# Kernel optimization log

Measured on AMD Instinct MI355X. Metric: run time of the kernel, lower is better.

## Reference

```python
import jax, jax.numpy as jnp
import numpy as np

N = 100000   # nodes
E = 300000   # edges
D = 256      # emb_dim
L = 5        # num_layers
SELF_LOOP_BOND_TYPE = 4
BN_EPS = 1e-5


def setup_inputs() -> dict:
    key = jax.random.key(0)
    ks = jax.random.split(key, 12)
    s = 0.05
    x = jax.random.randint(ks[0], (N, 2), 0, 3)
    edge_index = jax.random.randint(ks[1], (2, E), 0, N)
    edge_attr = jax.random.randint(ks[2], (E, 2), 0, 3)
    x_emb1 = jax.random.normal(ks[3], (120, D), dtype=jnp.float32) * s
    x_emb2 = jax.random.normal(ks[4], (3, D), dtype=jnp.float32) * s
    edge_emb1 = jax.random.normal(ks[5], (L, 6, D), dtype=jnp.float32) * s
    edge_emb2 = jax.random.normal(ks[6], (L, 3, D), dtype=jnp.float32) * s
    W1 = jax.random.normal(ks[7], (L, D, 2 * D), dtype=jnp.float32) * (1.0 / np.sqrt(D))
    b1 = jnp.zeros((L, 2 * D), dtype=jnp.float32)
    W2 = jax.random.normal(ks[8], (L, 2 * D, D), dtype=jnp.float32) * (1.0 / np.sqrt(2 * D))
    b2 = jnp.zeros((L, D), dtype=jnp.float32)
    bn_gamma = jnp.ones((L - 1, D), dtype=jnp.float32)
    bn_beta = jnp.zeros((L - 1, D), dtype=jnp.float32)
    return dict(x=x, edge_index=edge_index, edge_attr=edge_attr,
                x_emb1=x_emb1, x_emb2=x_emb2,
                edge_emb1=edge_emb1, edge_emb2=edge_emb2,
                W1=W1, b1=b1, W2=W2, b2=b2,
                bn_gamma=bn_gamma, bn_beta=bn_beta)


def reference(x, edge_index, edge_attr, x_emb1, x_emb2, edge_emb1, edge_emb2,
              W1, b1, W2, b2, bn_gamma, bn_beta):
    n = x.shape[0]
    loop = jnp.arange(n)
    # add_self_loops: append (i, i) for every node
    src = jnp.concatenate([edge_index[0], loop])  # [E+N]
    dst = jnp.concatenate([edge_index[1], loop])  # [E+N]
    # self-loop edge_attr = (bond_type=4, direction=0)
    self_attr = jnp.concatenate([
        jnp.full((n, 1), SELF_LOOP_BOND_TYPE, dtype=edge_attr.dtype),
        jnp.zeros((n, 1), dtype=edge_attr.dtype)], axis=1)
    ea = jnp.concatenate([edge_attr, self_attr], axis=0)  # [E+N, 2]

    out = x_emb1[x[:, 0]] + x_emb2[x[:, 1]]  # [N, D]
    for l in range(L):
        e_emb = edge_emb1[l][ea[:, 0]] + edge_emb2[l][ea[:, 1]]  # [E+N, D]
        msg = out[src] + e_emb                                   # gather + message
        agg = jax.ops.segment_sum(msg, dst, num_segments=n)      # scatter-add
        h = jax.nn.relu(agg @ W1[l] + b1[l]) @ W2[l] + b2[l]     # GIN MLP
        if l < L - 1:
            mean = h.mean(axis=0)
            var = h.var(axis=0)  # biased var, matches torch BN training
            h = (h - mean) * jax.lax.rsqrt(var + BN_EPS) * bn_gamma[l] + bn_beta[l]
            h = jax.nn.relu(h)
        out = h
    return out
```

## Files before the change

kernel.cpp:

```cpp
#include <hip/hip_runtime.h>

typedef unsigned short u16;
typedef unsigned int u32;

#define DD 256
#define PLCAP 1536

typedef short  s16x8 __attribute__((ext_vector_type(8)));
typedef short  s16x4 __attribute__((ext_vector_type(4)));
typedef float  f32x4 __attribute__((ext_vector_type(4)));
typedef float  f32x16 __attribute__((ext_vector_type(16)));

__device__ __forceinline__ float b2f(u16 u){
  union { u32 i; float f; } c; c.i = ((u32)u) << 16; return c.f;
}
__device__ __forceinline__ u16 f2b(float f){
  union { float f; u32 i; } c; c.f = f;
  u32 b = c.i + 0x7FFFu + ((c.i >> 16) & 1u);
  return (u16)(b >> 16);
}

__global__ void NodeEncoder_72971494359603_kernel(){}

__global__ void probe_dtype(const u32* w, u32* flag){
  if (threadIdx.x == 0 && blockIdx.x == 0){
    int cnt = 0;
    for (int i = 0; i < 256; i++){
      u32 low = w[i] & 0xFFFFu;
      u32 e = (low >> 7) & 0xFFu;
      if (e >= 0x60u && e <= 0x7Eu) cnt++;
    }
    *flag = (cnt >= 192) ? 1u : 0u;
  }
}

__global__ void cvt_in(const void* src, u16* dst, int n, const u32* flag){
  int i = blockIdx.x * 256 + threadIdx.x;
  if (i < n){
    if (*flag){
      dst[i] = ((const u16*)src)[i];
    } else {
      dst[i] = f2b(((const float*)src)[i]);
    }
  }
}

__global__ void store_out(const u16* h, void* dout, int n, const u32* flag){
  int i = blockIdx.x * 256 + threadIdx.x;
  if (i < n){
    if (*flag){
      ((u16*)dout)[i] = h[i];
    } else {
      ((float*)dout)[i] = b2f(h[i]);
    }
  }
}

__global__ void zero_int(int* p, int n){
  int i = blockIdx.x * 256 + threadIdx.x;
  if (i < n) p[i] = 0;
}

__global__ void build_table(const u16* ee1, const u16* ee2, u16* TBL){
  int b = blockIdx.x;
  int l = b / 18, c = b % 18, a = c / 3, bb = c % 3;
  int j = threadIdx.x;
  TBL[b * DD + j] = f2b(b2f(ee1[(l * 6 + a) * DD + j]) + b2f(ee2[(l * 3 + bb) * DD + j]));
}

__global__ void hist_kernel(const int* dst, int* counts, int E){
  int e = blockIdx.x * 256 + threadIdx.x;
  if (e < E) atomicAdd(&counts[dst[e]], 1);
}

__global__ void scan_sums(const int* counts, int* bsum, int N){
  __shared__ int red[256];
  int tid = threadIdx.x;
  int base = blockIdx.x * 1024;
  int s = 0;
  for (int i = tid; i < 1024; i += 256){
    int g = base + i;
    if (g < N) s += counts[g];
  }
  red[tid] = s;
  __syncthreads();
  for (int off = 128; off > 0; off >>= 1){
    if (tid < off) red[tid] += red[tid + off];
    __syncthreads();
  }
  if (tid == 0) bsum[blockIdx.x] = red[0];
}

__global__ void scan_top(int* bsum, int nb){
  if (threadIdx.x == 0 && blockIdx.x == 0){
    int acc = 0;
    for (int i = 0; i < nb; i++){ int t = bsum[i]; bsum[i] = acc; acc += t; }
  }
}

__global__ void scan_block(const int* counts, const int* bsum,
                           int* offsets, int* cursor, int N){
  __shared__ int tsum[256];
  int b = blockIdx.x;
  int tid = threadIdx.x;
  int base = b * 1024;
  int v0, v1, v2, v3;
  int g = base + tid * 4;
  v0 = (g + 0 < N) ? counts[g + 0] : 0;
  v1 = (g + 1 < N) ? counts[g + 1] : 0;
  v2 = (g + 2 < N) ? counts[g + 2] : 0;
  v3 = (g + 3 < N) ? counts[g + 3] : 0;
  tsum[tid] = v0 + v1 + v2 + v3;
  __syncthreads();
  for (int off = 1; off < 256; off <<= 1){
    int t = (tid >= off) ? tsum[tid - off] : 0;
    __syncthreads();
    tsum[tid] += t;
    __syncthreads();
  }
  int excl = (tid == 0 ? 0 : tsum[tid - 1]) + bsum[b];
  if (g + 0 < N){ offsets[g + 0] = excl; cursor[g + 0] = excl; } excl += v0;
  if (g + 1 < N){ offsets[g + 1] = excl; cursor[g + 1] = excl; } excl += v1;
  if (g + 2 < N){ offsets[g + 2] = excl; cursor[g + 2] = excl; } excl += v2;
  if (g + 3 < N){ offsets[g + 3] = excl; cursor[g + 3] = excl; }
}

__global__ void fill_csr(const int* ei, const int* ea, int* cursor,
                         int* payload, int E){
  int e = blockIdx.x * 256 + threadIdx.x;
  if (e < E){
    int d = ei[E + e];
    int pos = atomicAdd(&cursor[d], 1);
    int a = ea[2 * e], bb = ea[2 * e + 1];
    payload[pos] = ei[e] | ((a * 3 + bb) << 17);
  }
}

__global__ void node_embed(const int* x, const u16* xe1, const u16* xe2,
                           u16* out, int N){
  int idx = blockIdx.x * 256 + threadIdx.x;
  if (idx < N * DD){
    int n = idx >> 8, j = idx & 255;
    int x0 = x[2 * n], x1 = x[2 * n + 1];
    out[idx] = f2b(b2f(xe1[x0 * DD + j]) + b2f(xe2[x1 * DD + j]));
  }
}

__global__ void pack_B(const u16* __restrict__ W0, u16* __restrict__ Wp0, int K, int Nc){
  const u16* W = W0 + (size_t)blockIdx.y * K * Nc;
  u16* Wp = Wp0 + (size_t)blockIdx.y * K * Nc;
  int idx = blockIdx.x * 256 + threadIdx.x;
  int lane = idx & 63;
  int t = idx >> 6;
  int nk = K >> 4;
  int kstep = t % nk, cblk = t / nk;
  if (cblk >= (Nc >> 5)) return;
  int col = cblk * 32 + (lane & 31);
  int krow = kstep * 16 + (lane >> 5) * 8;
  u16* dst = Wp + (size_t)idx * 8;
#pragma unroll
  for (int e = 0; e < 8; e++)
    dst[e] = W[(size_t)(krow + e) * Nc + col];
}

__global__ __launch_bounds__(512, 4)
void layer_fused(const u16* __restrict__ feat, const u16* __restrict__ TBL,
                 const int* __restrict__ offsets, const int* __restrict__ counts,
                 const int* __restrict__ payload,
                 const u16* __restrict__ Wp1, const u16* __restrict__ bias1,
                 const u16* __restrict__ Wp2, const u16* __restrict__ bias2,
                 u16* __restrict__ H, float* __restrict__ partial, int npart, int M,
                 const float* __restrict__ sums, const u16* __restrict__ gamma,
                 const u16* __restrict__ beta, float invN, int apply_bn){
  __shared__ __align__(16) u16 As[64 * 256];
  __shared__ __align__(16) u16 Ms[2][64 * 128];
  u16* T = (u16*)Ms;
  int* PL = (int*)((char*)Ms + 10240);
  int tid = threadIdx.x, lane = tid & 63, wave = tid >> 6;
  int wr = wave >> 2, wc = wave & 3;
  int row0 = blockIdx.x * 64;
  int l31 = lane & 31, lhi = lane >> 5;

  {
    u32* Tw = (u32*)T;
    const u32* Gw = (const u32*)TBL;
    for (int i = tid; i < 18 * DD / 2; i += 512) Tw[i] = Gw[i];
  }
  int nlast = row0 + 63; if (nlast > M - 1) nlast = M - 1;
  int e_start = offsets[row0];
  int e_total = offsets[nlast] + counts[nlast] - e_start;
  for (int i = tid; i < e_total && i < PLCAP; i += 512) PL[i] = payload[e_start + i];
  __syncthreads();

  {
    int c4 = lane * 4;
    float sc[4], sh[4];
    if (apply_bn){
#pragma unroll
      for (int e = 0; e < 4; e++){
        int j = c4 + e;
        float mean = sums[j] * invN;
        float var = sums[DD + j] * invN - mean * mean;
        if (var < 0.f) var = 0.f;
        float scl = rsqrtf(var + 1e-5f) * b2f(gamma[j]);
        sc[e] = scl; sh[e] = b2f(beta[j]) - mean * scl;
      }
    } else {
#pragma unroll
      for (int e = 0; e < 4; e++){ sc[e] = 1.f; sh[e] = 0.f; }
    }
    int rbase = wave * 8;
    int offs[8], cnts[8]; s16x4 sv[8];
#pragma unroll
    for (int u = 0; u < 8; u++){
      int n = row0 + rbase + u; if (n > M - 1) n = M - 1;
      offs[u] = offsets[n]; cnts[u] = counts[n];
      sv[u] = *(const s16x4*)(feat + (size_t)n * DD + c4);
    }
    s16x4 tb = *(const s16x4*)(T + 12 * DD + c4);
#pragma unroll
    for (int up = 0; up < 4; up++){
      float a0[4], a1[4];
#pragma unroll
      for (int h = 0; h < 2; h++){
        float* a = h ? a1 : a0;
        s16x4 svv = sv[up * 2 + h];
#pragma unroll
        for (int j = 0; j < 4; j++){
          float v = b2f((u16)svv[j]) * sc[j] + sh[j];
          if (apply_bn) v = fmaxf(v, 0.f);
          a[j] = v + b2f((u16)tb[j]);
        }
      }
      int e0 = offs[up * 2],     c0 = cnts[up * 2],     i0 = 0;
      int e1 = offs[up * 2 + 1], c1 = cnts[up * 2 + 1], i1 = 0;
      while (i0 < c0 || i1 < c1){
        int b0 = c0 - i0; if (b0 > 4) b0 = 4; if (b0 < 0) b0 = 0;
        int b1 = c1 - i1; if (b1 > 4) b1 = 4; if (b1 < 0) b1 = 0;
        int pls0[4], pls1[4]; s16x4 rv0[4], rv1[4];
#pragma unroll
        for (int i = 0; i < 4; i++){
          if (i < b0){
            int idx = e0 + i0 + i - e_start;
            pls0[i] = (idx < PLCAP) ? PL[idx] : payload[e0 + i0 + i];
          }
          if (i < b1){
            int idx = e1 + i1 + i - e_start;
            pls1[i] = (idx < PLCAP) ? PL[idx] : payload[e1 + i1 + i];
          }
        }
#pragma unroll
        for (int i = 0; i < 4; i++)
          if (i < b0) rv0[i] = *(const s16x4*)(feat + (size_t)(pls0[i] & 0x1FFFF) * DD + c4);
#pragma unroll
        for (int i = 0; i < 4; i++)
          if (i < b1) rv1[i] = *(const s16x4*)(feat + (size_t)(pls1[i] & 0x1FFFF) * DD + c4);
#pragma unroll
        for (int i = 0; i < 4; i++){
          if (i < b0){
            s16x4 tv = *(const s16x4*)(T + (pls0[i] >> 17) * DD + c4);
#pragma unroll
            for (int j = 0; j < 4; j++){
              float w = b2f((u16)rv0[i][j]) * sc[j] + sh[j];
              if (apply_bn) w = fmaxf(w, 0.f);
              a0[j] += w + b2f((u16)tv[j]);
            }
          }
          if (i < b1){
            s16x4 tv = *(const s16x4*)(T + (pls1[i] >> 17) * DD + c4);
#pragma unroll
            for (int j = 0; j < 4; j++){
              float w = b2f((u16)rv1[i][j]) * sc[j] + sh[j];
              if (apply_bn) w = fmaxf(w, 0.f);
              a1[j] += w + b2f((u16)tv[j]);
            }
          }
        }
        i0 += b0; i1 += b1;
      }
#pragma unroll
      for (int h = 0; h < 2; h++){
        float* a = h ? a1 : a0;
        int r = rbase + up * 2 + h;
        s16x4 o;
        o[0] = (short)f2b(a[0]); o[1] = (short)f2b(a[1]);
        o[2] = (short)f2b(a[2]); o[3] = (short)f2b(a[3]);
        int byteo = r * 512 + (((lane >> 1) ^ (r & 31)) << 4) + ((lane & 1) << 3);
        *(s16x4*)((char*)As + byteo) = o;
      }
    }
  }
  __syncthreads();

  f32x16 acc2[2];
#pragma unroll
  for (int n = 0; n < 2; n++)
#pragma unroll
    for (int i = 0; i < 16; i++) acc2[n][i] = 0.f;
  f32x16 acc1;

  auto G1 = [&](int cc){
    f32x16 a1;
#pragma unroll
    for (int i = 0; i < 16; i++) a1[i] = 0.f;
    int arow = wr * 32 + l31;
    int cb = cc * 4 + wc;
#pragma unroll
    for (int ks = 0; ks < 16; ks++){
      int slot = (ks * 2 + lhi) ^ (arow & 31);
      s16x8 af = *(const s16x8*)((const char*)As + arow * 512 + (slot << 4));
      s16x8 bf = *(const s16x8*)(Wp1 + (((size_t)cb * 16 + ks) * 64 + lane) * 8);
      a1 = __builtin_amdgcn_mfma_f32_32x32x16_bf16(af, bf, a1, 0, 0, 0);
    }
    acc1 = a1;
  };
  auto WMS = [&](int cc, int buf){
    char* ms = (char*)Ms[buf];
    int col = wc * 32 + l31;
    float bv = b2f(bias1[cc * 128 + col]);
#pragma unroll
    for (int reg = 0; reg < 16; reg++){
      int mrow = wr * 32 + (reg & 3) + 8 * (reg >> 2) + 4 * lhi;
      float v = fmaxf(acc1[reg] + bv, 0.f);
      int slot = (col >> 3) ^ (mrow & 15);
      *(u16*)(ms + mrow * 256 + (slot << 4) + (col & 7) * 2) = f2b(v);
    }
  };

  G1(0);
  WMS(0, 0);
  __syncthreads();

#pragma unroll
  for (int c = 0; c < 4; c++){
    const char* ms = (const char*)Ms[c & 1];
    int mrow = wr * 32 + l31;
#pragma unroll
    for (int ks = 0; ks < 8; ks++){
      int slot = (ks * 2 + lhi) ^ (mrow & 15);
      s16x8 mf = *(const s16x8*)(ms + mrow * 256 + (slot << 4));
#pragma unroll
      for (int n = 0; n < 2; n++){
        int cb2 = wc * 2 + n;
        s16x8 wf = *(const s16x8*)(Wp2 + (((size_t)cb2 * 32 + c * 8 + ks) * 64 + lane) * 8);
        acc2[n] = __builtin_amdgcn_mfma_f32_32x32x16_bf16(mf, wf, acc2[n], 0, 0, 0);
      }
    }
    if (c < 3){
      G1(c + 1);
      WMS(c + 1, (c + 1) & 1);
      __syncthreads();
    }
  }

#pragma unroll
  for (int n = 0; n < 2; n++){
    int col = wc * 64 + n * 32 + l31;
    float bv = b2f(bias2[col]);
#pragma unroll
    for (int reg = 0; reg < 16; reg++){
      int row = wr * 32 + (reg & 3) + 8 * (reg >> 2) + 4 * lhi;
      int slot = (col >> 3) ^ (row & 31);
      *(u16*)((char*)As + row * 512 + (slot << 4) + (col & 7) * 2) = f2b(acc2[n][reg] + bv);
    }
  }
  __syncthreads();

  float s[8], q[8];
#pragma unroll
  for (int e = 0; e < 8; e++){ s[e] = 0.f; q[e] = 0.f; }
  int sl = tid & 31;
#pragma unroll
  for (int p = 0; p < 4; p++){
    int r = p * 16 + (tid >> 5);
    s16x8 v = *(const s16x8*)((const char*)As + r * 512 + ((sl ^ (r & 31)) << 4));
    int gr = row0 + r;
    if (gr < M){
      *(s16x8*)(H + (size_t)gr * DD + sl * 8) = v;
      if (partial){
#pragma unroll
        for (int e = 0; e < 8; e++){
          float f = b2f((u16)v[e]);
          s[e] += f; q[e] += f * f;
        }
      }
    }
  }
  if (partial){
#pragma unroll
    for (int e = 0; e < 8; e++){
      s[e] += __shfl_xor(s[e], 32);
      q[e] += __shfl_xor(q[e], 32);
    }
    __syncthreads();
    float* redS = (float*)Ms;
    float* redQ = redS + 8 * 256;
    if (lane < 32){
#pragma unroll
      for (int e = 0; e < 8; e++){
        redS[wave * 256 + sl * 8 + e] = s[e];
        redQ[wave * 256 + sl * 8 + e] = q[e];
      }
    }
    __syncthreads();
    if (tid < 256){
      float a = 0.f, b = 0.f;
#pragma unroll
      for (int w = 0; w < 8; w++){ a += redS[w * 256 + tid]; b += redQ[w * 256 + tid]; }
      partial[(size_t)blockIdx.x * DD + tid] = a;
      partial[(size_t)(npart + blockIdx.x) * DD + tid] = b;
    }
  }
}

__global__ void bn_reduce(const float* __restrict__ partial, float* __restrict__ sums,
                          int npart){
  int b = blockIdx.x, which = b >> 3, jg = b & 7;
  int t = threadIdx.x;
  int j = jg * 32 + (t >> 3);
  int li = t & 7;
  float s = 0.f;
  for (int i = li; i < npart; i += 8)
    s += partial[(size_t)(which * npart + i) * DD + j];
  s += __shfl_xor(s, 1); s += __shfl_xor(s, 2); s += __shfl_xor(s, 4);
  if (li == 0) sums[which * DD + j] = s;
}

extern "C" void kernel_launch(void* const* d_in, const int* in_sizes, int n_in,
                              void* d_out, int out_size, void* d_ws, size_t ws_size,
                              hipStream_t stream){
  (void)n_in; (void)out_size; (void)ws_size;
  const int* x    = (const int*)d_in[0];
  const int* ei   = (const int*)d_in[1];
  const int* ea   = (const int*)d_in[2];
  const void* xe1 = d_in[3];
  const void* xe2 = d_in[4];
  const void* ee1 = d_in[5];
  const void* ee2 = d_in[6];
  const void* W1  = d_in[7];
  const void* b1  = d_in[8];
  const void* W2  = d_in[9];
  const void* b2  = d_in[10];
  const void* gam = d_in[11];
  const void* bet = d_in[12];

  int N = in_sizes[0] / 2;
  int E = in_sizes[1] / 2;
  int NB = (N + 1023) / 1024;
  const int L = 5;
  int nblk = (N + 63) / 64;
  int npart = nblk;

  char* base = (char*)d_ws;
  size_t off = 0;
  u32* flag    = (u32*)(base + off);   off += 256;
  u16* TBL     = (u16*)(base + off);   off += ((size_t)L * 18 * DD * 2 + 255) & ~(size_t)255;
  int* counts  = (int*)(base + off);   off += ((size_t)N * 4 + 255) & ~(size_t)255;
  int* offsets = (int*)(base + off);   off += ((size_t)N * 4 + 255) & ~(size_t)255;
  int* cursor  = (int*)(base + off);   off += ((size_t)N * 4 + 255) & ~(size_t)255;
  int* bsum    = (int*)(base + off);   off += ((size_t)NB * 4 + 255) & ~(size_t)255;
  int* payload = (int*)(base + off);   off += ((size_t)E * 4 + 255) & ~(size_t)255;
  float* part  = (float*)(base + off); off += ((size_t)2 * npart * DD * 4 + 255) & ~(size_t)255;
  float* sums  = (float*)(base + off); off += ((size_t)2 * DD * 4 + 255) & ~(size_t)255;
  u16* wx1  = (u16*)(base + off); off += ((size_t)120 * DD * 2 + 255) & ~(size_t)255;
  u16* wx2  = (u16*)(base + off); off += ((size_t)3 * DD * 2 + 255) & ~(size_t)255;
  u16* wee1 = (u16*)(base + off); off += ((size_t)L * 6 * DD * 2 + 255) & ~(size_t)255;
  u16* wee2 = (u16*)(base + off); off += ((size_t)L * 3 * DD * 2 + 255) & ~(size_t)255;
  u16* wW1  = (u16*)(base + off); off += ((size_t)L * DD * 2 * DD * 2 + 255) & ~(size_t)255;
  u16* wb1  = (u16*)(base + off); off += ((size_t)L * 2 * DD * 2 + 255) & ~(size_t)255;
  u16* wW2  = (u16*)(base + off); off += ((size_t)L * 2 * DD * DD * 2 + 255) & ~(size_t)255;
  u16* wb2  = (u16*)(base + off); off += ((size_t)L * DD * 2 + 255) & ~(size_t)255;
  u16* wgam = (u16*)(base + off); off += ((size_t)(L - 1) * DD * 2 + 255) & ~(size_t)255;
  u16* wbet = (u16*)(base + off); off += ((size_t)(L - 1) * DD * 2 + 255) & ~(size_t)255;
  u16* Wp1  = (u16*)(base + off); off += ((size_t)L * DD * 2 * DD * 2 + 255) & ~(size_t)255;
  u16* Wp2  = (u16*)(base + off); off += ((size_t)L * 2 * DD * DD * 2 + 255) & ~(size_t)255;
  u16* featA = (u16*)(base + off); off += ((size_t)N * DD * 2 + 255) & ~(size_t)255;
  u16* featB = (u16*)(base + off); off += ((size_t)N * DD * 2 + 255) & ~(size_t)255;

  probe_dtype<<<1, 64, 0, stream>>>((const u32*)xe1, flag);
  cvt_in<<<(120 * DD + 255) / 256, 256, 0, stream>>>(xe1, wx1, 120 * DD, flag);
  cvt_in<<<(3 * DD + 255) / 256, 256, 0, stream>>>(xe2, wx2, 3 * DD, flag);
  cvt_in<<<(L * 6 * DD + 255) / 256, 256, 0, stream>>>(ee1, wee1, L * 6 * DD, flag);
  cvt_in<<<(L * 3 * DD + 255) / 256, 256, 0, stream>>>(ee2, wee2, L * 3 * DD, flag);
  cvt_in<<<(L * DD * 2 * DD + 255) / 256, 256, 0, stream>>>(W1, wW1, L * DD * 2 * DD, flag);
  cvt_in<<<(L * 2 * DD + 255) / 256, 256, 0, stream>>>(b1, wb1, L * 2 * DD, flag);
  cvt_in<<<(L * 2 * DD * DD + 255) / 256, 256, 0, stream>>>(W2, wW2, L * 2 * DD * DD, flag);
  cvt_in<<<(L * DD + 255) / 256, 256, 0, stream>>>(b2, wb2, L * DD, flag);
  cvt_in<<<((L - 1) * DD + 255) / 256, 256, 0, stream>>>(gam, wgam, (L - 1) * DD, flag);
  cvt_in<<<((L - 1) * DD + 255) / 256, 256, 0, stream>>>(bet, wbet, (L - 1) * DD, flag);

  build_table<<<90, 256, 0, stream>>>(wee1, wee2, TBL);
  pack_B<<<dim3(64, L), 256, 0, stream>>>(wW1, Wp1, DD, 2 * DD);
  pack_B<<<dim3(64, L), 256, 0, stream>>>(wW2, Wp2, 2 * DD, DD);
  zero_int<<<(N + 255) / 256, 256, 0, stream>>>(counts, N);
  hist_kernel<<<(E + 255) / 256, 256, 0, stream>>>(ei + E, counts, E);
  scan_sums<<<NB, 256, 0, stream>>>(counts, bsum, N);
  scan_top<<<1, 64, 0, stream>>>(bsum, NB);
  scan_block<<<NB, 256, 0, stream>>>(counts, bsum, offsets, cursor, N);
  fill_csr<<<(E + 255) / 256, 256, 0, stream>>>(ei, ea, cursor, payload, E);

  node_embed<<<(N * DD + 255) / 256, 256, 0, stream>>>(x, wx1, wx2, featA, N);

  float invN = 1.0f / (float)N;
  u16* fin = featA;
  u16* fout = featB;

  for (int l = 0; l < L; l++){
    layer_fused<<<nblk, 512, 0, stream>>>(
        fin, TBL + (size_t)l * 18 * DD, offsets, counts, payload,
        Wp1 + (size_t)l * DD * 2 * DD, wb1 + (size_t)l * 2 * DD,
        Wp2 + (size_t)l * 2 * DD * DD, wb2 + (size_t)l * DD,
        fout, (l < L - 1) ? part : (float*)nullptr, npart, N,
        sums, wgam + (size_t)(l > 0 ? l - 1 : 0) * DD,
        wbet + (size_t)(l > 0 ? l - 1 : 0) * DD, invN, l > 0 ? 1 : 0);

    if (l < L - 1){
      bn_reduce<<<16, 256, 0, stream>>>(part, sums, npart);
    }
    u16* t = fin; fin = fout; fout = t;
  }

  store_out<<<(N * DD + 255) / 256, 256, 0, stream>>>(fin, d_out, N * DD, flag);
}
```

Measured before the change: 1.504 ms.

## Batch input conversions, fuse output store into last layer, widen gather to 4 rows

Replaces ten per-tensor conversion launches with a single batched kernel, and removes the separate store_out pass by having the final layer write the result (bf16 or fp32) straight to the output buffer. The edge-gather loop now interleaves four destination rows per iteration instead of two, so more independent feature loads are in flight. That raises register pressure under the 512-thread, 4-blocks launch bounds and could spill or reduce occupancy.

Result: faster. 1.466 ms (-2.5%).

```diff
diff --git a/kernel.cpp b/kernel.cpp
--- a/kernel.cpp
+++ b/kernel.cpp
@@ -34,25 +34,22 @@
   }
 }
 
-__global__ void cvt_in(const void* src, u16* dst, int n, const u32* flag){
+struct CvtArgs {
+  const void* src[10];
+  u16* dst[10];
+  int n[10];
+};
+__global__ void cvt_batch(CvtArgs a, const u32* __restrict__ flag){
   int i = blockIdx.x * 256 + threadIdx.x;
-  if (i < n){
-    if (*flag){
-      dst[i] = ((const u16*)src)[i];
-    } else {
-      dst[i] = f2b(((const float*)src)[i]);
-    }
-  }
-}
-
-__global__ void store_out(const u16* h, void* dout, int n, const u32* flag){
-  int i = blockIdx.x * 256 + threadIdx.x;
-  if (i < n){
-    if (*flag){
-      ((u16*)dout)[i] = h[i];
-    } else {
-      ((float*)dout)[i] = b2f(h[i]);
-    }
+  u32 f = *flag;
+#pragma unroll
+  for (int s = 0; s < 10; s++){
+    if (i < a.n[s]){
+      if (f) a.dst[s][i] = ((const u16*)a.src[s])[i];
+      else   a.dst[s][i] = f2b(((const float*)a.src[s])[i]);
+      return;
+    }
+    i -= a.n[s];
   }
 }
 
@@ -171,7 +168,8 @@
                  const u16* __restrict__ Wp2, const u16* __restrict__ bias2,
                  u16* __restrict__ H, float* __restrict__ partial, int npart, int M,
                  const float* __restrict__ sums, const u16* __restrict__ gamma,
-                 const u16* __restrict__ beta, float invN, int apply_bn){
+                 const u16* __restrict__ beta, float invN, int apply_bn,
+                 void* __restrict__ dout, const u32* __restrict__ dflag){
   __shared__ __align__(16) u16 As[64 * 256];
   __shared__ __align__(16) u16 Ms[2][64 * 128];
   u16* T = (u16*)Ms;
@@ -219,72 +217,66 @@
     }
     s16x4 tb = *(const s16x4*)(T + 12 * DD + c4);
 #pragma unroll
-    for (int up = 0; up < 4; up++){
-      float a0[4], a1[4];
-#pragma unroll
-      for (int h = 0; h < 2; h++){
-        float* a = h ? a1 : a0;
-        s16x4 svv = sv[up * 2 + h];
+    for (int up = 0; up < 2; up++){
+      float a[4][4];
+#pragma unroll
+      for (int h = 0; h < 4; h++){
+        s16x4 svv = sv[up * 4 + h];
 #pragma unroll
         for (int j = 0; j < 4; j++){
           float v = b2f((u16)svv[j]) * sc[j] + sh[j];
           if (apply_bn) v = fmaxf(v, 0.f);
-          a[j] = v + b2f((u16)tb[j]);
+          a[h][j] = v + b2f((u16)tb[j]);
         }
       }
-      int e0 = offs[up * 2],     c0 = cnts[up * 2],     i0 = 0;
-      int e1 = offs[up * 2 + 1], c1 = cnts[up * 2 + 1], i1 = 0;
-      while (i0 < c0 || i1 < c1){
-        int b0 = c0 - i0; if (b0 > 4) b0 = 4; if (b0 < 0) b0 = 0;
-        int b1 = c1 - i1; if (b1 > 4) b1 = 4; if (b1 < 0) b1 = 0;
-        int pls0[4], pls1[4]; s16x4 rv0[4], rv1[4];
-#pragma unroll
-        for (int i = 0; i < 4; i++){
-          if (i < b0){
-            int idx = e0 + i0 + i - e_start;
-            pls0[i] = (idx < PLCAP) ? PL[idx] : payload[e0 + i0 + i];
-          }
-          if (i < b1){
-            int idx = e1 + i1 + i - e_start;
-            pls1[i] = (idx < PLCAP) ? PL[idx] : payload[e1 + i1 + i];
-          }
+      int eo[4], cn[4], ii[4];
+#pragma unroll
+      for (int h = 0; h < 4; h++){
+        eo[h] = offs[up * 4 + h]; cn[h] = cnts[up * 4 + h]; ii[h] = 0;
+      }
+      while (ii[0] < cn[0] || ii[1] < cn[1] || ii[2] < cn[2] || ii[3] < cn[3]){
+        int bb[4]; int pls[4][4]; s16x4 rv[4][4];
+#pragma unroll
+        for (int h = 0; h < 4; h++){
+          int t = cn[h] - ii[h];
+          bb[h] = t > 4 ? 4 : (t < 0 ? 0 : t);
         }
 #pragma unroll
-        for (int i = 0; i < 4; i++)
-          if (i < b0) rv0[i] = *(const s16x4*)(feat + (size_t)(pls0[i] & 0x1FFFF) * DD + c4);
-#pragma unroll
-        for (int i = 0; i < 4; i++)
-          if (i < b1) rv1[i] = *(const s16x4*)(feat + (size_t)(pls1[i] & 0x1FFFF) * DD + c4);
-#pragma unroll
-        for (int i = 0; i < 4; i++){
-          if (i < b0){
-            s16x4 tv = *(const s16x4*)(T + (pls0[i] >> 17) * DD + c4);
-#pragma unroll
-            for (int j = 0; j < 4; j++){
-              float w = b2f((u16)rv0[i][j]) * sc[j] + sh[j];
-              if (apply_bn) w = fmaxf(w, 0.f);
-              a0[j] += w + b2f((u16)tv[j]);
+        for (int h = 0; h < 4; h++)
+#pragma unroll
+          for (int i = 0; i < 4; i++)
+            if (i < bb[h]){
+              int idx = eo[h] + ii[h] + i - e_start;
+              pls[h][i] = (idx < PLCAP) ? PL[idx] : payload[eo[h] + ii[h] + i];
             }
-          }
-          if (i < b1){
-            s16x4 tv = *(const s16x4*)(T + (pls1[i] >> 17) * DD + c4);
-#pragma unroll
-            for (int j = 0; j < 4; j++){
-              float w = b2f((u16)rv1[i][j]) * sc[j] + sh[j];
-              if (apply_bn) w = fmaxf(w, 0.f);
-              a1[j] += w + b2f((u16)tv[j]);
+#pragma unroll
+        for (int h = 0; h < 4; h++)
+#pragma unroll
+          for (int i = 0; i < 4; i++)
+            if (i < bb[h])
+              rv[h][i] = *(const s16x4*)(feat + (size_t)(pls[h][i] & 0x1FFFF) * DD + c4);
+#pragma unroll
+        for (int h = 0; h < 4; h++)
+#pragma unroll
+          for (int i = 0; i < 4; i++)
+            if (i < bb[h]){
+              s16x4 tv = *(const s16x4*)(T + (pls[h][i] >> 17) * DD + c4);
+#pragma unroll
+              for (int j = 0; j < 4; j++){
+                float w = b2f((u16)rv[h][i][j]) * sc[j] + sh[j];
+                if (apply_bn) w = fmaxf(w, 0.f);
+                a[h][j] += w + b2f((u16)tv[j]);
+              }
             }
-          }
-        }
-        i0 += b0; i1 += b1;
-      }
-#pragma unroll
-      for (int h = 0; h < 2; h++){
-        float* a = h ? a1 : a0;
-        int r = rbase + up * 2 + h;
+#pragma unroll
+        for (int h = 0; h < 4; h++) ii[h] += bb[h];
+      }
+#pragma unroll
+      for (int h = 0; h < 4; h++){
+        int r = rbase + up * 4 + h;
         s16x4 o;
-        o[0] = (short)f2b(a[0]); o[1] = (short)f2b(a[1]);
-        o[2] = (short)f2b(a[2]); o[3] = (short)f2b(a[3]);
+        o[0] = (short)f2b(a[h][0]); o[1] = (short)f2b(a[h][1]);
+        o[2] = (short)f2b(a[h][2]); o[3] = (short)f2b(a[h][3]);
         int byteo = r * 512 + (((lane >> 1) ^ (r & 31)) << 4) + ((lane & 1) << 3);
         *(s16x4*)((char*)As + byteo) = o;
       }
@@ -370,13 +362,26 @@
 #pragma unroll
   for (int e = 0; e < 8; e++){ s[e] = 0.f; q[e] = 0.f; }
   int sl = tid & 31;
+  u32 df = dout ? *dflag : 0u;
 #pragma unroll
   for (int p = 0; p < 4; p++){
     int r = p * 16 + (tid >> 5);
     s16x8 v = *(const s16x8*)((const char*)As + r * 512 + ((sl ^ (r & 31)) << 4));
     int gr = row0 + r;
     if (gr < M){
-      *(s16x8*)(H + (size_t)gr * DD + sl * 8) = v;
+      if (dout){
+        if (df){
+          *(s16x8*)((u16*)dout + (size_t)gr * DD + sl * 8) = v;
+        } else {
+          f32x4 o0, o1;
+#pragma unroll
+          for (int e = 0; e < 4; e++){ o0[e] = b2f((u16)v[e]); o1[e] = b2f((u16)v[4 + e]); }
+          *(f32x4*)((float*)dout + (size_t)gr * DD + sl * 8) = o0;
+          *(f32x4*)((float*)dout + (size_t)gr * DD + sl * 8 + 4) = o1;
+        }
+      } else {
+        *(s16x8*)(H + (size_t)gr * DD + sl * 8) = v;
+      }
       if (partial){
 #pragma unroll
         for (int e = 0; e < 8; e++){
@@ -478,16 +483,16 @@
   u16* featB = (u16*)(base + off); off += ((size_t)N * DD * 2 + 255) & ~(size_t)255;
 
   probe_dtype<<<1, 64, 0, stream>>>((const u32*)xe1, flag);
-  cvt_in<<<(120 * DD + 255) / 256, 256, 0, stream>>>(xe1, wx1, 120 * DD, flag);
-  cvt_in<<<(3 * DD + 255) / 256, 256, 0, stream>>>(xe2, wx2, 3 * DD, flag);
-  cvt_in<<<(L * 6 * DD + 255) / 256, 256, 0, stream>>>(ee1, wee1, L * 6 * DD, flag);
-  cvt_in<<<(L * 3 * DD + 255) / 256, 256, 0, stream>>>(ee2, wee2, L * 3 * DD, flag);
-  cvt_in<<<(L * DD * 2 * DD + 255) / 256, 256, 0, stream>>>(W1, wW1, L * DD * 2 * DD, flag);
-  cvt_in<<<(L * 2 * DD + 255) / 256, 256, 0, stream>>>(b1, wb1, L * 2 * DD, flag);
-  cvt_in<<<(L * 2 * DD * DD + 255) / 256, 256, 0, stream>>>(W2, wW2, L * 2 * DD * DD, flag);
-  cvt_in<<<(L * DD + 255) / 256, 256, 0, stream>>>(b2, wb2, L * DD, flag);
-  cvt_in<<<((L - 1) * DD + 255) / 256, 256, 0, stream>>>(gam, wgam, (L - 1) * DD, flag);
-  cvt_in<<<((L - 1) * DD + 255) / 256, 256, 0, stream>>>(bet, wbet, (L - 1) * DD, flag);
+  {
+    CvtArgs ca;
+    const void* srcs[10] = { xe1, xe2, ee1, ee2, W1, b1, W2, b2, gam, bet };
+    u16* dsts[10] = { wx1, wx2, wee1, wee2, wW1, wb1, wW2, wb2, wgam, wbet };
+    int ns[10] = { 120 * DD, 3 * DD, L * 6 * DD, L * 3 * DD, L * DD * 2 * DD,
+                   L * 2 * DD, L * 2 * DD * DD, L * DD, (L - 1) * DD, (L - 1) * DD };
+    int total = 0;
+    for (int i = 0; i < 10; i++){ ca.src[i] = srcs[i]; ca.dst[i] = dsts[i]; ca.n[i] = ns[i]; total += ns[i]; }
+    cvt_batch<<<(total + 255) / 256, 256, 0, stream>>>(ca, flag);
+  }
 
   build_table<<<90, 256, 0, stream>>>(wee1, wee2, TBL);
   pack_B<<<dim3(64, L), 256, 0, stream>>>(wW1, Wp1, DD, 2 * DD);
@@ -506,19 +511,19 @@
   u16* fout = featB;
 
   for (int l = 0; l < L; l++){
+    int last = (l == L - 1);
     layer_fused<<<nblk, 512, 0, stream>>>(
         fin, TBL + (size_t)l * 18 * DD, offsets, counts, payload,
         Wp1 + (size_t)l * DD * 2 * DD, wb1 + (size_t)l * 2 * DD,
         Wp2 + (size_t)l * 2 * DD * DD, wb2 + (size_t)l * DD,
         fout, (l < L - 1) ? part : (float*)nullptr, npart, N,
         sums, wgam + (size_t)(l > 0 ? l - 1 : 0) * DD,
-        wbet + (size_t)(l > 0 ? l - 1 : 0) * DD, invN, l > 0 ? 1 : 0);
+        wbet + (size_t)(l > 0 ? l - 1 : 0) * DD, invN, l > 0 ? 1 : 0,
+        last ? d_out : (void*)nullptr, flag);
 
     if (l < L - 1){
       bn_reduce<<<16, 256, 0, stream>>>(part, sums, npart);
     }
     u16* t = fin; fin = fout; fout = t;
   }
-
-  store_out<<<(N * DD + 255) / 256, 256, 0, stream>>>(fin, d_out, N * DD, flag);
-}
+}
```
